# Optimization experiments

Hardware: AMD Instinct MI355X
Metric: run time of the kernel (lower is better)

Reference implementation:

```python
import jax, jax.numpy as jnp
import numpy as np
from jax import lax

BITS = 8
CLIP = 2.0 ** (BITS - 1) - 1.0  # 127 for int8 symmetric quantization
EPS = 1e-6


def _quantize(x):
    """Dynamic per-tensor symmetric quantization (AQT-style).

    Returns the integer-valued (but float-dtype) quantized tensor and the
    scale such that dequant = q / scale.
    """
    bound = jnp.maximum(jnp.max(jnp.abs(x)), EPS)
    scale = CLIP / bound
    q = jnp.clip(jnp.round(x * scale), -CLIP, CLIP)
    return q, scale


def setup_inputs() -> dict:
    key = jax.random.key(0)
    k1, k2 = jax.random.split(key)
    lhs = jax.random.normal(k1, (4096, 4096), dtype=jnp.float32)
    rhs = jax.random.normal(k2, (4096, 4096), dtype=jnp.float32)
    return {"lhs": lhs, "rhs": rhs}


def reference(lhs, rhs):
    # Quantize both operands with dynamically computed per-tensor scales,
    # do the matmul on the integer-valued tensors, then dequantize the
    # result by the product of scales. This is the math aqt_ops.aqt_dot
    q_lhs, s_lhs = _quantize(lhs)
    q_rhs, s_rhs = _quantize(rhs)
    acc = jnp.matmul(q_lhs, q_rhs)  # [M, N], integer-valued accumulation
    return acc / (s_lhs * s_rhs)
```

## Files before the change

kernel.cpp:

```cpp
#include <hip/hip_runtime.h>
#include <hip/hip_bf16.h>


typedef int v4i __attribute__((ext_vector_type(4)));

#define MAT_N 4096

__device__ __forceinline__ void async_copy16(const void* g, void* l) {
    __builtin_amdgcn_global_load_lds(
        (const __attribute__((address_space(1))) void*)g,
        (__attribute__((address_space(3))) void*)l,
        16, 0, 0);
}

__device__ __forceinline__ unsigned uabs_bits(float f) {
    return __float_as_uint(f) & 0x7fffffffu;
}

__global__ __launch_bounds__(256) void absmax2_kernel(
    const float4* __restrict__ lhs, const float4* __restrict__ rhs,
    unsigned* __restrict__ slots) {
    const float4* x = lhs;
    unsigned* slot = slots;
    int b = blockIdx.x;
    if (b >= 2048) { x = rhs; slot = slots + 1; b -= 2048; }
    unsigned m0 = 0, m1 = 0, m2 = 0, m3 = 0;
    int i = b * 256 + threadIdx.x;
#pragma unroll
    for (int u = 0; u < 8; u++, i += 524288) {
        float4 v = x[i];
        m0 = max(m0, uabs_bits(v.x));
        m1 = max(m1, uabs_bits(v.y));
        m2 = max(m2, uabs_bits(v.z));
        m3 = max(m3, uabs_bits(v.w));
    }
    unsigned m = max(max(m0, m1), max(m2, m3));
#pragma unroll
    for (int off = 32; off > 0; off >>= 1)
        m = max(m, (unsigned)__shfl_down(m, off, 64));
    __shared__ unsigned sm[4];
    if ((threadIdx.x & 63) == 0) sm[threadIdx.x >> 6] = m;
    __syncthreads();
    if (threadIdx.x == 0) {
        m = max(max(sm[0], sm[1]), max(sm[2], sm[3]));
        atomicMax(slot, m);
    }
}

__global__ __launch_bounds__(256) void quant_fused_kernel(
    const float* __restrict__ lhs, const float* __restrict__ rhs,
    unsigned char* __restrict__ qA, signed char* __restrict__ qBT,
    const unsigned* __restrict__ slots) {
    const int N = MAT_N;
    const int t = threadIdx.x;
    __shared__ __align__(16) signed char smT[64 * 80];

    int b = blockIdx.x;
    if (b < 4096) {
        const float s = 127.0f / fmaxf(__uint_as_float(slots[0]), 1e-6f);
        const float4* x4 = (const float4*)lhs;
        unsigned* q4 = (unsigned*)qA;
        const int base4 = b * 1024;
#pragma unroll
        for (int u = 0; u < 4; u++) {
            int idx = base4 + u * 256 + t;
            float4 v = x4[idx];
            int a = min(127, max(-127, (int)rintf(v.x * s)));
            int bq = min(127, max(-127, (int)rintf(v.y * s)));
            int c = min(127, max(-127, (int)rintf(v.z * s)));
            int d = min(127, max(-127, (int)rintf(v.w * s)));
            q4[idx] = (unsigned)(a & 0xff) | ((unsigned)(bq & 0xff) << 8) |
                      ((unsigned)(c & 0xff) << 16) | ((unsigned)(d & 0xff) << 24);
        }
    } else {
        const float s = 127.0f / fmaxf(__uint_as_float(slots[1]), 1e-6f);
        b -= 4096;
        const int n0 = (b & 63) * 64;
        const int k0 = (b >> 6) * 64;
        const int mk = t >> 4;
        const int mn = t & 15;
        const float4* x4 = (const float4*)rhs;

        unsigned w[4];
#pragma unroll
        for (int i = 0; i < 4; i++) {
            float4 v = x4[(size_t)(k0 + 4 * mk + i) * (N / 4) + (n0 >> 2) + mn];
            int a = min(127, max(-127, (int)rintf(v.x * s)));
            int bq = min(127, max(-127, (int)rintf(v.y * s)));
            int c = min(127, max(-127, (int)rintf(v.z * s)));
            int d = min(127, max(-127, (int)rintf(v.w * s)));
            w[i] = (unsigned)(a & 0xff) | ((unsigned)(bq & 0xff) << 8) |
                   ((unsigned)(c & 0xff) << 16) | ((unsigned)(d & 0xff) << 24);
        }
#pragma unroll
        for (int j = 0; j < 4; j++) {
            unsigned selj = (unsigned)j | ((unsigned)(4 + j) << 8) |
                            ((unsigned)j << 16) | ((unsigned)(4 + j) << 24);
            unsigned p01 = __builtin_amdgcn_perm(w[1], w[0], selj);
            unsigned p23 = __builtin_amdgcn_perm(w[3], w[2], selj);
            unsigned uj = __builtin_amdgcn_perm(p23, p01, 0x05040100u);
            *(unsigned*)(smT + (4 * mn + j) * 80 + 4 * mk) = uj;
        }
        __syncthreads();
        const int nr = t >> 2;
        const int kq = (t & 3) * 16;
        int4 val = *(const int4*)(smT + nr * 80 + kq);
        *(int4*)(qBT + (size_t)(n0 + nr) * N + k0 + kq) = val;
    }
}

__global__ __launch_bounds__(256) void gemm_i8_kernel(
    const signed char* __restrict__ A, const signed char* __restrict__ BT,
    float* __restrict__ C, const unsigned* __restrict__ slots) {
    const int N = MAT_N;
    __shared__ __align__(16) signed char As[128 * 128];
    __shared__ __align__(16) signed char Bs[128 * 128];

    const int tid = threadIdx.x;
    const int wave = tid >> 6;
    const int lane = tid & 63;
    const int quad = lane >> 4;
    const int mrow = lane & 15;
    const int wr = (wave >> 1) * 64;
    const int wc = (wave & 1) * 64;
    const int brow = blockIdx.y * 128;
    const int bcol = blockIdx.x * 128;

    v4i acc[4][4] = {};

    int gaoff[4], gboff[4];
    signed char* la[4];
    signed char* lb[4];
#pragma unroll
    for (int u = 0; u < 4; u++) {
        int c = tid + 256 * u;
        int r = c >> 3;
        int q = (c & 7) ^ (r & 7);
        gaoff[u] = (brow + r) * N + q * 16;
        gboff[u] = (bcol + r) * N + q * 16;
        la[u] = As + c * 16;
        lb[u] = Bs + c * 16;
    }

    for (int k0 = 0; k0 < N; k0 += 128) {
        __syncthreads();
#pragma unroll
        for (int u = 0; u < 4; u++) async_copy16(A + gaoff[u] + k0, la[u]);
#pragma unroll
        for (int u = 0; u < 4; u++) async_copy16(BT + gboff[u] + k0, lb[u]);
        __syncthreads();

#pragma unroll
        for (int s = 0; s < 2; s++) {
            const int kq = s * 4 + quad;
            v4i af[4], bf[4];
#pragma unroll
            for (int i = 0; i < 4; i++) {
                int r = wr + i * 16 + mrow;
                af[i] = *(const v4i*)(As + (r * 8 + (kq ^ (r & 7))) * 16);
            }
#pragma unroll
            for (int j = 0; j < 4; j++) {
                int r = wc + j * 16 + mrow;
                bf[j] = *(const v4i*)(Bs + (r * 8 + (kq ^ (r & 7))) * 16);
            }
#pragma unroll
            for (int i = 0; i < 4; i++)
#pragma unroll
                for (int j = 0; j < 4; j++)
                    acc[i][j] = __builtin_amdgcn_mfma_i32_16x16x64_i8(
                        af[i], bf[j], acc[i][j], 0, 0, 0);
        }
    }

    const float bl = fmaxf(__uint_as_float(slots[0]), 1e-6f);
    const float br = fmaxf(__uint_as_float(slots[1]), 1e-6f);
    const float dq = bl * br * (1.0f / (127.0f * 127.0f));

#pragma unroll
    for (int i = 0; i < 4; i++) {
        const int row0 = brow + wr + i * 16 + quad * 4;
#pragma unroll
        for (int j = 0; j < 4; j++) {
            const int col = bcol + wc + j * 16 + mrow;
#pragma unroll
            for (int r = 0; r < 4; r++)
                C[(size_t)(row0 + r) * N + col] = (float)acc[i][j][r] * dq;
        }
    }
}

extern "C" void kernel_launch(void* const* d_in, const int* in_sizes, int n_in,
                              void* d_out, int out_size, void* d_ws, size_t ws_size,
                              hipStream_t stream) {
    const float* lhs = (const float*)d_in[0];
    const float* rhs = (const float*)d_in[1];
    float* out = (float*)d_out;

    unsigned* slots = (unsigned*)d_ws;
    signed char* qA = (signed char*)d_ws + 256;
    signed char* qBT = qA + (size_t)MAT_N * MAT_N;

    hipMemsetAsync(d_ws, 0, 8, stream);
    absmax2_kernel<<<4096, 256, 0, stream>>>(
        (const float4*)lhs, (const float4*)rhs, slots);
    quant_fused_kernel<<<8192, 256, 0, stream>>>(
        lhs, rhs, (unsigned char*)qA, qBT, slots);
    gemm_i8_kernel<<<dim3(32, 32), 256, 0, stream>>>(qA, qBT, out, slots);
}
```

Baseline: 278.1 us.

## Use 32x32 int8 MFMA, swizzled block order, and two-stage absmax without atomics

The absmax pass now writes per-block partial maxima instead of atomics, which removes the memset launch. Each block of the quant and GEMM kernels re-reduces those partials itself. The GEMM switches from 16x16x64 to 32x32x32 int8 MFMA with a 2x2 accumulator tile per wave. It also gets a modified LDS XOR swizzle and an 8x8 supertile block remap for L2 reuse. The redundant per-block reductions and the changed output store pattern add some overhead.

```diff
diff --git a/kernel.cpp b/kernel.cpp
--- a/kernel.cpp
+++ b/kernel.cpp
@@ -3,6 +3,7 @@
 
 
 typedef int v4i __attribute__((ext_vector_type(4)));
+typedef int v16i __attribute__((ext_vector_type(16)));
 
 #define MAT_N 4096
 
@@ -17,18 +18,16 @@
     return __float_as_uint(f) & 0x7fffffffu;
 }
 
-__global__ __launch_bounds__(256) void absmax2_kernel(
+__global__ __launch_bounds__(256) void absmax_partial_kernel(
     const float4* __restrict__ lhs, const float4* __restrict__ rhs,
-    unsigned* __restrict__ slots) {
-    const float4* x = lhs;
-    unsigned* slot = slots;
-    int b = blockIdx.x;
-    if (b >= 2048) { x = rhs; slot = slots + 1; b -= 2048; }
+    unsigned* __restrict__ pmax) {
+    const int b = blockIdx.x;
+    const float4* x = (b < 512) ? lhs : rhs;
+    const float4* p = x + (size_t)(b & 511) * 8192;
     unsigned m0 = 0, m1 = 0, m2 = 0, m3 = 0;
-    int i = b * 256 + threadIdx.x;
-#pragma unroll
-    for (int u = 0; u < 8; u++, i += 524288) {
-        float4 v = x[i];
+#pragma unroll 8
+    for (int u = 0; u < 32; u++) {
+        float4 v = p[u * 256 + threadIdx.x];
         m0 = max(m0, uabs_bits(v.x));
         m1 = max(m1, uabs_bits(v.y));
         m2 = max(m2, uabs_bits(v.z));
@@ -41,23 +40,36 @@
     __shared__ unsigned sm[4];
     if ((threadIdx.x & 63) == 0) sm[threadIdx.x >> 6] = m;
     __syncthreads();
-    if (threadIdx.x == 0) {
-        m = max(max(sm[0], sm[1]), max(sm[2], sm[3]));
-        atomicMax(slot, m);
-    }
+    if (threadIdx.x == 0)
+        pmax[b] = max(max(sm[0], sm[1]), max(sm[2], sm[3]));
 }
 
 __global__ __launch_bounds__(256) void quant_fused_kernel(
     const float* __restrict__ lhs, const float* __restrict__ rhs,
     unsigned char* __restrict__ qA, signed char* __restrict__ qBT,
-    const unsigned* __restrict__ slots) {
+    const unsigned* __restrict__ pmax) {
     const int N = MAT_N;
     const int t = threadIdx.x;
+    int b = blockIdx.x;
     __shared__ __align__(16) signed char smT[64 * 80];
-
-    int b = blockIdx.x;
+    __shared__ unsigned red[4];
+    __shared__ float s_sh;
+
+    const int slot0 = (b < 4096) ? 0 : 512;
+    unsigned mm = max(pmax[slot0 + t], pmax[slot0 + 256 + t]);
+#pragma unroll
+    for (int off = 32; off > 0; off >>= 1)
+        mm = max(mm, (unsigned)__shfl_down(mm, off, 64));
+    if ((t & 63) == 0) red[t >> 6] = mm;
+    __syncthreads();
+    if (t == 0) {
+        unsigned f = max(max(red[0], red[1]), max(red[2], red[3]));
+        s_sh = 127.0f / fmaxf(__uint_as_float(f), 1e-6f);
+    }
+    __syncthreads();
+    const float s = s_sh;
+
     if (b < 4096) {
-        const float s = 127.0f / fmaxf(__uint_as_float(slots[0]), 1e-6f);
         const float4* x4 = (const float4*)lhs;
         unsigned* q4 = (unsigned*)qA;
         const int base4 = b * 1024;
@@ -73,7 +85,6 @@
                       ((unsigned)(c & 0xff) << 16) | ((unsigned)(d & 0xff) << 24);
         }
     } else {
-        const float s = 127.0f / fmaxf(__uint_as_float(slots[1]), 1e-6f);
         b -= 4096;
         const int n0 = (b & 63) * 64;
         const int k0 = (b >> 6) * 64;
@@ -111,7 +122,7 @@
 
 __global__ __launch_bounds__(256) void gemm_i8_kernel(
     const signed char* __restrict__ A, const signed char* __restrict__ BT,
-    float* __restrict__ C, const unsigned* __restrict__ slots) {
+    float* __restrict__ C, const unsigned* __restrict__ pmax) {
     const int N = MAT_N;
     __shared__ __align__(16) signed char As[128 * 128];
     __shared__ __align__(16) signed char Bs[128 * 128];
@@ -119,14 +130,20 @@
     const int tid = threadIdx.x;
     const int wave = tid >> 6;
     const int lane = tid & 63;
-    const int quad = lane >> 4;
-    const int mrow = lane & 15;
+    const int m32 = lane & 31;
+    const int h = lane >> 5;
     const int wr = (wave >> 1) * 64;
     const int wc = (wave & 1) * 64;
-    const int brow = blockIdx.y * 128;
-    const int bcol = blockIdx.x * 128;
-
-    v4i acc[4][4] = {};
+
+    const int flat = blockIdx.x;
+    const int super = flat >> 6;
+    const int within = flat & 63;
+    const int bx = (super & 3) * 8 + (within & 7);
+    const int by = (super >> 2) * 8 + (within >> 3);
+    const int brow = by * 128;
+    const int bcol = bx * 128;
+
+    v16i acc[2][2] = {};
 
     int gaoff[4], gboff[4];
     signed char* la[4];
@@ -135,13 +152,24 @@
     for (int u = 0; u < 4; u++) {
         int c = tid + 256 * u;
         int r = c >> 3;
-        int q = (c & 7) ^ (r & 7);
+        int q = (c & 7) ^ ((r ^ (r >> 3)) & 7);
         gaoff[u] = (brow + r) * N + q * 16;
         gboff[u] = (bcol + r) * N + q * 16;
         la[u] = As + c * 16;
         lb[u] = Bs + c * 16;
     }
 
+    int abase[2], avr[2], bbase[2], bvr[2];
+#pragma unroll
+    for (int i = 0; i < 2; i++) {
+        int r = wr + i * 32 + m32;
+        abase[i] = r * 8;
+        avr[i] = (r ^ (r >> 3)) & 7;
+        r = wc + i * 32 + m32;
+        bbase[i] = r * 8;
+        bvr[i] = (r ^ (r >> 3)) & 7;
+    }
+
     for (int k0 = 0; k0 < N; k0 += 128) {
         __syncthreads();
 #pragma unroll
@@ -151,43 +179,52 @@
         __syncthreads();
 
 #pragma unroll
-        for (int s = 0; s < 2; s++) {
-            const int kq = s * 4 + quad;
-            v4i af[4], bf[4];
-#pragma unroll
-            for (int i = 0; i < 4; i++) {
-                int r = wr + i * 16 + mrow;
-                af[i] = *(const v4i*)(As + (r * 8 + (kq ^ (r & 7))) * 16);
+        for (int s = 0; s < 4; s++) {
+            const int q = 2 * s + h;
+            v4i af[2], bf[2];
+#pragma unroll
+            for (int i = 0; i < 2; i++)
+                af[i] = *(const v4i*)(As + (abase[i] + (q ^ avr[i])) * 16);
+#pragma unroll
+            for (int j = 0; j < 2; j++)
+                bf[j] = *(const v4i*)(Bs + (bbase[j] + (q ^ bvr[j])) * 16);
+#pragma unroll
+            for (int i = 0; i < 2; i++)
+#pragma unroll
+                for (int j = 0; j < 2; j++)
+                    acc[i][j] = __builtin_amdgcn_mfma_i32_32x32x32_i8(
+                        af[i], bf[j], acc[i][j], 0, 0, 0);
+        }
+    }
+
+    __shared__ unsigned redl[4], redr[4];
+    unsigned ml = max(pmax[tid], pmax[tid + 256]);
+    unsigned mr = max(pmax[512 + tid], pmax[768 + tid]);
+#pragma unroll
+    for (int off = 32; off > 0; off >>= 1) {
+        ml = max(ml, (unsigned)__shfl_down(ml, off, 64));
+        mr = max(mr, (unsigned)__shfl_down(mr, off, 64));
+    }
+    if (lane == 0) { redl[wave] = ml; redr[wave] = mr; }
+    __syncthreads();
+    const float bl = fmaxf(
+        __uint_as_float(max(max(redl[0], redl[1]), max(redl[2], redl[3]))), 1e-6f);
+    const float br = fmaxf(
+        __uint_as_float(max(max(redr[0], redr[1]), max(redr[2], redr[3]))), 1e-6f);
+    const float dq = bl * br * (1.0f / (127.0f * 127.0f));
+
+#pragma unroll
+    for (int i = 0; i < 2; i++)
+#pragma unroll
+        for (int j = 0; j < 2; j++) {
+            const int col = bcol + wc + j * 32 + m32;
+#pragma unroll
+            for (int reg = 0; reg < 16; reg++) {
+                const int row =
+                    brow + wr + i * 32 + (reg & 3) + 8 * (reg >> 2) + 4 * h;
+                C[(size_t)row * N + col] = (float)acc[i][j][reg] * dq;
             }
-#pragma unroll
-            for (int j = 0; j < 4; j++) {
-                int r = wc + j * 16 + mrow;
-                bf[j] = *(const v4i*)(Bs + (r * 8 + (kq ^ (r & 7))) * 16);
-            }
-#pragma unroll
-            for (int i = 0; i < 4; i++)
-#pragma unroll
-                for (int j = 0; j < 4; j++)
-                    acc[i][j] = __builtin_amdgcn_mfma_i32_16x16x64_i8(
-                        af[i], bf[j], acc[i][j], 0, 0, 0);
-        }
-    }
-
-    const float bl = fmaxf(__uint_as_float(slots[0]), 1e-6f);
-    const float br = fmaxf(__uint_as_float(slots[1]), 1e-6f);
-    const float dq = bl * br * (1.0f / (127.0f * 127.0f));
-
-#pragma unroll
-    for (int i = 0; i < 4; i++) {
-        const int row0 = brow + wr + i * 16 + quad * 4;
-#pragma unroll
-        for (int j = 0; j < 4; j++) {
-            const int col = bcol + wc + j * 16 + mrow;
-#pragma unroll
-            for (int r = 0; r < 4; r++)
-                C[(size_t)(row0 + r) * N + col] = (float)acc[i][j][r] * dq;
-        }
-    }
+        }
 }
 
 extern "C" void kernel_launch(void* const* d_in, const int* in_sizes, int n_in,
@@ -197,14 +234,13 @@
     const float* rhs = (const float*)d_in[1];
     float* out = (float*)d_out;
 
-    unsigned* slots = (unsigned*)d_ws;
-    signed char* qA = (signed char*)d_ws + 256;
+    unsigned* pmax = (unsigned*)d_ws;
+    signed char* qA = (signed char*)d_ws + 8192;
     signed char* qBT = qA + (size_t)MAT_N * MAT_N;
 
-    hipMemsetAsync(d_ws, 0, 8, stream);
-    absmax2_kernel<<<4096, 256, 0, stream>>>(
-        (const float4*)lhs, (const float4*)rhs, slots);
+    absmax_partial_kernel<<<1024, 256, 0, stream>>>(
+        (const float4*)lhs, (const float4*)rhs, pmax);
     quant_fused_kernel<<<8192, 256, 0, stream>>>(
-        lhs, rhs, (unsigned char*)qA, qBT, slots);
-    gemm_i8_kernel<<<dim3(32, 32), 256, 0, stream>>>(qA, qBT, out, slots);
-}
+        lhs, rhs, (unsigned char*)qA, qBT, pmax);
+    gemm_i8_kernel<<<1024, 256, 0, stream>>>(qA, qBT, out, pmax);
+}
```

New measurement: 260.0 us. 6.5% less time.
